# Kernel optimization log

Measured on AMD Instinct MI355X. Metric: run time of the kernel, lower is better.

Reference implementation:

```python
import jax, jax.numpy as jnp
import numpy as np

N_NODES = 50000
N_EDGES = 800000
D_IN, D_HID, D_OUT = 128, 256, 128


def setup_inputs() -> dict:
    key = jax.random.key(0)
    ks = jax.random.split(key, 8)
    x = jax.random.normal(ks[0], (N_NODES, D_IN), dtype=jnp.float32)
    edge_index = jax.random.randint(ks[1], (2, N_EDGES), 0, N_NODES, dtype=jnp.int64)
    # Xavier-ish scale for stability
    W_l1 = jax.random.normal(ks[2], (D_HID, D_IN), dtype=jnp.float32) * (1.0 / np.sqrt(D_IN))
    b_l1 = jnp.zeros((D_HID,), dtype=jnp.float32)
    W_r1 = jax.random.normal(ks[3], (D_HID, D_IN), dtype=jnp.float32) * (1.0 / np.sqrt(D_IN))
    W_l2 = jax.random.normal(ks[4], (D_OUT, D_HID), dtype=jnp.float32) * (1.0 / np.sqrt(D_HID))
    b_l2 = jnp.zeros((D_OUT,), dtype=jnp.float32)
    W_r2 = jax.random.normal(ks[5], (D_OUT, D_HID), dtype=jnp.float32) * (1.0 / np.sqrt(D_HID))
    return {"x": x, "edge_index": edge_index, "W_l1": W_l1, "b_l1": b_l1,
            "W_r1": W_r1, "W_l2": W_l2, "b_l2": b_l2, "W_r2": W_r2}


def _sage_conv(x, src, dst, W_l, b_l, W_r):
    # SAGEConv (aggr='mean', root_weight=True, normalize=False):
    #   out_i = W_l @ mean_{j in N(i)} x_j + b_l + W_r @ x_i
    n = x.shape[0]
    msgs = x[src]                                             # [E, d] gather
    agg = jax.ops.segment_sum(msgs, dst, num_segments=n)      # [N, d] scatter-add
    deg = jax.ops.segment_sum(jnp.ones((src.shape[0],), x.dtype), dst,
                              num_segments=n)
    agg = agg / jnp.maximum(deg, 1.0)[:, None]                # mean (0 for isolated)
    return agg @ W_l.T + b_l + x @ W_r.T


def reference(x, edge_index, W_l1, b_l1, W_r1, W_l2, b_l2, W_r2):
    # Note: PyG BasicGNN with num_layers=1 and jk=None applies NO activation
    # after its single conv, so the stack is two bare SAGEConv layers.
    src, dst = edge_index[0], edge_index[1]
    h = _sage_conv(x, src, dst, W_l1, b_l1, W_r1)
    out = _sage_conv(h, src, dst, W_l2, b_l2, W_r2)
    return out
```

## Files before the change

### kernel.cpp

```cpp
#include <hip/hip_runtime.h>

typedef __attribute__((ext_vector_type(4))) float f32x4;
typedef __attribute__((ext_vector_type(8))) short bf16x8;

__device__ inline ushort f2bf(float f) {
    uint u = __builtin_bit_cast(uint, f);
    u += 0x7fff + ((u >> 16) & 1);
    return (ushort)(u >> 16);
}
__device__ inline float bf2f(ushort h) {
    uint u = ((uint)h) << 16;
    return __builtin_bit_cast(float, u);
}

#define GRP 8
#define NSLICE 6250
#define CHUNK 2048

__global__ __launch_bounds__(256) void k_hist_p(const int* __restrict__ ei,
                                                int* __restrict__ cnt, int nE) {
    const int g = blockIdx.x & 7;
    const int c = blockIdx.x >> 3;
    const int lo = g * NSLICE, hi = lo + NSLICE;
    #pragma unroll
    for (int p = 0; p < CHUNK / 256; ++p) {
        int e = c * CHUNK + p * 256 + threadIdx.x;
        if (e < nE) {
            int d = ei[nE + e];
            if (d >= lo && d < hi) atomicAdd(&cnt[d], 1);
        }
    }
}

__global__ __launch_bounds__(1024) void k_scan1(const int* __restrict__ cnt,
                                                int* __restrict__ rp,
                                                int* __restrict__ bsum, int n) {
    __shared__ int buf[1024];
    const int tid = threadIdx.x;
    const int i = blockIdx.x * 1024 + tid;
    int v = (i < n) ? cnt[i] : 0;
    buf[tid] = v;
    __syncthreads();
    #pragma unroll
    for (int off = 1; off < 1024; off <<= 1) {
        int t = 0;
        if (tid >= off) t = buf[tid - off];
        __syncthreads();
        if (tid >= off) buf[tid] += t;
        __syncthreads();
    }
    if (i < n) rp[i] = buf[tid] - v;
    if (tid == 1023) bsum[blockIdx.x] = buf[1023];
}

__global__ void k_scan2(const int* __restrict__ bsum, int* __restrict__ bofs,
                        int* __restrict__ rp, int nb, int n) {
    if (threadIdx.x == 0 && blockIdx.x == 0) {
        int run = 0;
        for (int b = 0; b < nb; ++b) { bofs[b] = run; run += bsum[b]; }
        rp[n] = run;
    }
}

__global__ __launch_bounds__(1024) void k_scan3(int* __restrict__ rp,
                                                const int* __restrict__ bofs, int n) {
    int i = blockIdx.x * 1024 + threadIdx.x;
    if (i < n) rp[i] += bofs[blockIdx.x];
}

__global__ __launch_bounds__(256) void k_fill_p(const int* __restrict__ ei,
                                                const int* __restrict__ rp,
                                                int* __restrict__ cur,
                                                int* __restrict__ srt, int nE) {
    const int g = blockIdx.x & 7;
    const int c = blockIdx.x >> 3;
    const int lo = g * NSLICE, hi = lo + NSLICE;
    #pragma unroll
    for (int p = 0; p < CHUNK / 256; ++p) {
        int e = c * CHUNK + p * 256 + threadIdx.x;
        if (e < nE) {
            int d = ei[nE + e];
            int s = ei[e];
            if (d >= lo && d < hi) {
                int pos = rp[d] + atomicAdd(&cur[d], 1);
                srt[pos] = s;
            }
        }
    }
}

__global__ __launch_bounds__(256) void k_cvt_x(const float* __restrict__ x,
                                               ushort* __restrict__ A1, int n) {
    int e4 = blockIdx.x * 256 + threadIdx.x;
    if (e4 >= n * 32) return;
    int i = e4 >> 5, c4 = e4 & 31;
    float4 v = *(const float4*)(x + (size_t)i * 128 + c4 * 4);
    ushort4 o;
    o.x = f2bf(v.x); o.y = f2bf(v.y); o.z = f2bf(v.z); o.w = f2bf(v.w);
    *(ushort4*)(A1 + (size_t)i * 256 + 128 + c4 * 4) = o;
}

__global__ __launch_bounds__(256) void k_cvt_w(
    const float* __restrict__ Wl1, const float* __restrict__ Wr1,
    const float* __restrict__ Wl2, const float* __restrict__ Wr2,
    ushort* __restrict__ W1cat, ushort* __restrict__ W2cat) {
    int t = blockIdx.x * 256 + threadIdx.x;
    int which = t >> 14;
    int r = (t >> 6) & 255;
    int kq = t & 63;
    const float* src;
    ushort* dst;
    if (which == 0) {
        src = (kq < 32) ? (Wl1 + (size_t)r * 128 + kq * 4)
                        : (Wr1 + (size_t)r * 128 + (kq - 32) * 4);
        dst = W1cat + (size_t)r * 256 + kq * 4;
    } else {
        src = (r < 128) ? (Wl2 + (size_t)r * 256 + kq * 4)
                        : (Wr2 + (size_t)(r - 128) * 256 + kq * 4);
        dst = W2cat + (size_t)r * 256 + kq * 4;
    }
    float4 v = *(const float4*)src;
    ushort4 o;
    o.x = f2bf(v.x); o.y = f2bf(v.y); o.z = f2bf(v.z); o.w = f2bf(v.w);
    *(ushort4*)dst = o;
}

__global__ __launch_bounds__(256) void k_gather1(ushort* A1,
                                                 const int* __restrict__ srt,
                                                 const int* __restrict__ rp, int n) {
    const int node = blockIdx.x * 4 + (threadIdx.x >> 6);
    if (node >= n) return;
    const int lane = threadIdx.x & 63;
    const int beg = rp[node], end = rp[node + 1];
    float ax = 0.f, ay = 0.f;
    int e = beg;
    for (; e + 7 < end; e += 8) {
        uint v[8];
        #pragma unroll
        for (int q = 0; q < 8; ++q)
            v[q] = *(const uint*)(A1 + (size_t)srt[e + q] * 256 + 128 + lane * 2);
        #pragma unroll
        for (int q = 0; q < 8; ++q) {
            ax += bf2f((ushort)v[q]);
            ay += bf2f((ushort)(v[q] >> 16));
        }
    }
    for (; e < end; ++e) {
        uint v0 = *(const uint*)(A1 + (size_t)srt[e] * 256 + 128 + lane * 2);
        ax += bf2f((ushort)v0);
        ay += bf2f((ushort)(v0 >> 16));
    }
    const float invd = 1.0f / fmaxf((float)(end - beg), 1.0f);
    uint o = ((uint)f2bf(ay * invd) << 16) | (uint)f2bf(ax * invd);
    *(uint*)(A1 + (size_t)node * 256 + lane * 2) = o;
}

__global__ __launch_bounds__(256) void k_gather2(const ushort* __restrict__ H2,
                                                 const int* __restrict__ srt,
                                                 const int* __restrict__ rp,
                                                 const float* __restrict__ b2,
                                                 float* __restrict__ out, int n) {
    const int node = blockIdx.x * 4 + (threadIdx.x >> 6);
    if (node >= n) return;
    const int lane = threadIdx.x & 63;
    const int beg = rp[node], end = rp[node + 1];
    float ax = 0.f, ay = 0.f;
    int e = beg;
    for (; e + 7 < end; e += 8) {
        uint v[8];
        #pragma unroll
        for (int q = 0; q < 8; ++q)
            v[q] = *(const uint*)(H2 + (size_t)srt[e + q] * 256 + lane * 2);
        #pragma unroll
        for (int q = 0; q < 8; ++q) {
            ax += bf2f((ushort)v[q]);
            ay += bf2f((ushort)(v[q] >> 16));
        }
    }
    for (; e < end; ++e) {
        uint v0 = *(const uint*)(H2 + (size_t)srt[e] * 256 + lane * 2);
        ax += bf2f((ushort)v0);
        ay += bf2f((ushort)(v0 >> 16));
    }
    const float invd = 1.0f / fmaxf((float)(end - beg), 1.0f);
    uint rv = *(const uint*)(H2 + (size_t)node * 256 + 128 + lane * 2);
    float2 bb = *(const float2*)(b2 + lane * 2);
    float2 res;
    res.x = ax * invd + bf2f((ushort)rv) + bb.x;
    res.y = ay * invd + bf2f((ushort)(rv >> 16)) + bb.y;
    *(float2*)(out + (size_t)node * 128 + lane * 2) = res;
}

__global__ __launch_bounds__(512, 4) void k_gemm_fused(
    const ushort* __restrict__ A, const ushort* __restrict__ W1,
    const ushort* __restrict__ W2, const float* __restrict__ b1,
    ushort* __restrict__ O, int n)
{
    __shared__ __align__(16) char sA[32768];
    __shared__ __align__(16) char sH[32768];
    const int bi = blockIdx.x * 64;
    const int tid = threadIdx.x;

    #pragma unroll
    for (int p = 0; p < 4; ++p) {
        const int o = p * 8192 + tid * 16;
        const int row = o >> 9;
        const int cb = o & 511;
        uint4 v = *(const uint4*)((const char*)A + (size_t)(bi + row) * 512 + cb);
        *(uint4*)(sA + row * 512 + (cb ^ ((row & 7) << 4))) = v;
    }
    __syncthreads();

    const int wid = tid >> 6;
    const int lane = tid & 63;
    const int wn = wid * 32;
    const int lr = lane & 15;
    const int lkb = (lane >> 4) * 16;
    const int crow0 = (lane >> 4) * 4;
    const int ccol = lane & 15;

    {
        f32x4 acc[4][2] = {};
        #pragma unroll
        for (int kk = 0; kk < 8; ++kk) {
            bf16x8 wf[2], af[4];
            #pragma unroll
            for (int ni = 0; ni < 2; ++ni)
                wf[ni] = *(const bf16x8*)((const char*)W1 + (size_t)(wn + ni * 16 + lr) * 512 + kk * 64 + lkb);
            #pragma unroll
            for (int mi = 0; mi < 4; ++mi) {
                const int row = mi * 16 + lr;
                af[mi] = *(const bf16x8*)(sA + row * 512 + ((kk * 64 + lkb) ^ ((row & 7) << 4)));
            }
            #pragma unroll
            for (int mi = 0; mi < 4; ++mi)
                #pragma unroll
                for (int ni = 0; ni < 2; ++ni)
                    acc[mi][ni] = __builtin_amdgcn_mfma_f32_16x16x32_bf16(
                        af[mi], wf[ni], acc[mi][ni], 0, 0, 0);
        }
        const float badd0 = b1[wn + ccol];
        const float badd1 = b1[wn + 16 + ccol];
        #pragma unroll
        for (int mi = 0; mi < 4; ++mi)
            #pragma unroll
            for (int ni = 0; ni < 2; ++ni) {
                const int col = wn + ni * 16 + ccol;
                const float badd = ni ? badd1 : badd0;
                #pragma unroll
                for (int j = 0; j < 4; ++j) {
                    const int row = mi * 16 + crow0 + j;
                    *(ushort*)(sH + row * 512 + ((col * 2) ^ ((row & 7) << 4))) =
                        f2bf(acc[mi][ni][j] + badd);
                }
            }
    }
    __syncthreads();

    {
        f32x4 acc[4][2] = {};
        #pragma unroll
        for (int kk = 0; kk < 8; ++kk) {
            bf16x8 wf[2], af[4];
            #pragma unroll
            for (int ni = 0; ni < 2; ++ni)
                wf[ni] = *(const bf16x8*)((const char*)W2 + (size_t)(wn + ni * 16 + lr) * 512 + kk * 64 + lkb);
            #pragma unroll
            for (int mi = 0; mi < 4; ++mi) {
                const int row = mi * 16 + lr;
                af[mi] = *(const bf16x8*)(sH + row * 512 + ((kk * 64 + lkb) ^ ((row & 7) << 4)));
            }
            #pragma unroll
            for (int mi = 0; mi < 4; ++mi)
                #pragma unroll
                for (int ni = 0; ni < 2; ++ni)
                    acc[mi][ni] = __builtin_amdgcn_mfma_f32_16x16x32_bf16(
                        af[mi], wf[ni], acc[mi][ni], 0, 0, 0);
        }
        #pragma unroll
        for (int mi = 0; mi < 4; ++mi)
            #pragma unroll
            for (int ni = 0; ni < 2; ++ni) {
                const int ocol = wn + ni * 16 + ccol;
                #pragma unroll
                for (int j = 0; j < 4; ++j) {
                    const int grow = bi + mi * 16 + crow0 + j;
                    if (grow < n)
                        O[(size_t)grow * 256 + ocol] = f2bf(acc[mi][ni][j]);
                }
            }
    }
}

extern "C" void kernel_launch(void* const* d_in, const int* in_sizes, int n_in,
                              void* d_out, int out_size, void* d_ws, size_t ws_size,
                              hipStream_t stream) {
    const float* x   = (const float*)d_in[0];
    const int*   ei  = (const int*)  d_in[1];
    const float* Wl1 = (const float*)d_in[2];
    const float* bl1 = (const float*)d_in[3];
    const float* Wr1 = (const float*)d_in[4];
    const float* Wl2 = (const float*)d_in[5];
    const float* bl2 = (const float*)d_in[6];
    const float* Wr2 = (const float*)d_in[7];
    float* out = (float*)d_out;

    const int nN = 50000;
    const int nE = in_sizes[1] / 2;

    char* ws = (char*)d_ws;
    int*    rp    = (int*)   (ws);
    int*    cnt   = (int*)   (ws + 262144);
    int*    cur   = (int*)   (ws + 524288);
    int*    bsum  = (int*)   (ws + 786432);
    int*    bofs  = (int*)   (ws + 790528);
    int*    srt   = (int*)   (ws + (size_t)1 * (1 << 20));
    ushort* W1cat = (ushort*)(ws + (size_t)5 * (1 << 20));
    ushort* W2cat = (ushort*)(ws + (size_t)5 * (1 << 20) + 256 * 1024);
    ushort* A1    = (ushort*)(ws + (size_t)6 * (1 << 20));
    ushort* H2    = (ushort*)(ws + (size_t)32 * (1 << 20));

    const int nb = (nN + 1023) / 1024;
    const int nChunks = (nE + CHUNK - 1) / CHUNK;

    hipMemsetAsync(ws + 262144, 0, 462144, stream);
    k_hist_p<<<nChunks * GRP, 256, 0, stream>>>(ei, cnt, nE);
    k_scan1<<<nb, 1024, 0, stream>>>(cnt, rp, bsum, nN);
    k_scan2<<<1, 64, 0, stream>>>(bsum, bofs, rp, nb, nN);
    k_scan3<<<nb, 1024, 0, stream>>>(rp, bofs, nN);
    k_fill_p<<<nChunks * GRP, 256, 0, stream>>>(ei, rp, cur, srt, nE);

    k_cvt_x<<<(nN * 32 + 255) / 256, 256, 0, stream>>>(x, A1, nN);
    k_cvt_w<<<128, 256, 0, stream>>>(Wl1, Wr1, Wl2, Wr2, W1cat, W2cat);

    k_gather1<<<(nN + 3) / 4, 256, 0, stream>>>(A1, srt, rp, nN);
    k_gemm_fused<<<(nN + 63) / 64, 512, 0, stream>>>(A1, W1cat, W2cat, bl1, H2, nN);

    k_gather2<<<(nN + 3) / 4, 256, 0, stream>>>(H2, srt, rp, bl2, out, nN);
}
```

Baseline: 294.5 us.

## Fuse preprocessing kernels, merge scans, widen gathers, and share GEMM LDS buffer

Merges x/weight conversion and the histogram into one launch, and folds the serial block-offset scan into the add pass using a wave shuffle scan. The gathers now have each lane load 16 bytes and process four edges per wave-iteration, with cross-quad shuffle reductions. The fused GEMM reuses one LDS buffer for both stages so occupancy can rise from 4 to 6 blocks. The fill kernel loads the source index only when the edge is in range. These changes aim to cut launch overhead, serial scan latency and memory transaction count, at the cost of extra shuffles and masked lanes for low-degree nodes.

```diff
diff --git a/kernel.cpp b/kernel.cpp
--- a/kernel.cpp
+++ b/kernel.cpp
@@ -12,15 +12,59 @@
     uint u = ((uint)h) << 16;
     return __builtin_bit_cast(float, u);
 }
+__device__ inline uint packbf(float lo, float hi) {
+    return (uint)f2bf(lo) | ((uint)f2bf(hi) << 16);
+}
 
 #define GRP 8
 #define NSLICE 6250
 #define CHUNK 2048
 
-__global__ __launch_bounds__(256) void k_hist_p(const int* __restrict__ ei,
-                                                int* __restrict__ cnt, int nE) {
-    const int g = blockIdx.x & 7;
-    const int c = blockIdx.x >> 3;
+__global__ __launch_bounds__(256) void k_pre(
+    const float* __restrict__ x,
+    const float* __restrict__ Wl1, const float* __restrict__ Wr1,
+    const float* __restrict__ Wl2, const float* __restrict__ Wr2,
+    const int* __restrict__ ei,
+    ushort* __restrict__ A1, ushort* __restrict__ W1cat, ushort* __restrict__ W2cat,
+    int* __restrict__ cnt, int n, int nE, int nxb, int histBase)
+{
+    const int b = blockIdx.x;
+    if (b < nxb) {
+        int e4 = b * 256 + threadIdx.x;
+        if (e4 >= n * 32) return;
+        int i = e4 >> 5, c4 = e4 & 31;
+        float4 v = *(const float4*)(x + (size_t)i * 128 + c4 * 4);
+        ushort4 o;
+        o.x = f2bf(v.x); o.y = f2bf(v.y); o.z = f2bf(v.z); o.w = f2bf(v.w);
+        *(ushort4*)(A1 + (size_t)i * 256 + 128 + c4 * 4) = o;
+        return;
+    }
+    if (b < nxb + 128) {
+        int t = (b - nxb) * 256 + threadIdx.x;
+        int which = t >> 14;
+        int r = (t >> 6) & 255;
+        int kq = t & 63;
+        const float* src;
+        ushort* dst;
+        if (which == 0) {
+            src = (kq < 32) ? (Wl1 + (size_t)r * 128 + kq * 4)
+                            : (Wr1 + (size_t)r * 128 + (kq - 32) * 4);
+            dst = W1cat + (size_t)r * 256 + kq * 4;
+        } else {
+            src = (r < 128) ? (Wl2 + (size_t)r * 256 + kq * 4)
+                            : (Wr2 + (size_t)(r - 128) * 256 + kq * 4);
+            dst = W2cat + (size_t)r * 256 + kq * 4;
+        }
+        float4 v = *(const float4*)src;
+        ushort4 o;
+        o.x = f2bf(v.x); o.y = f2bf(v.y); o.z = f2bf(v.z); o.w = f2bf(v.w);
+        *(ushort4*)dst = o;
+        return;
+    }
+    if (b < histBase) return;
+    const int hb = b - histBase;
+    const int g = hb & 7;
+    const int c = hb >> 3;
     const int lo = g * NSLICE, hi = lo + NSLICE;
     #pragma unroll
     for (int p = 0; p < CHUNK / 256; ++p) {
@@ -53,19 +97,25 @@
     if (tid == 1023) bsum[blockIdx.x] = buf[1023];
 }
 
-__global__ void k_scan2(const int* __restrict__ bsum, int* __restrict__ bofs,
-                        int* __restrict__ rp, int nb, int n) {
-    if (threadIdx.x == 0 && blockIdx.x == 0) {
-        int run = 0;
-        for (int b = 0; b < nb; ++b) { bofs[b] = run; run += bsum[b]; }
-        rp[n] = run;
-    }
-}
-
-__global__ __launch_bounds__(1024) void k_scan3(int* __restrict__ rp,
-                                                const int* __restrict__ bofs, int n) {
+__global__ __launch_bounds__(1024) void k_scan3b(int* __restrict__ rp,
+                                                 const int* __restrict__ bsum,
+                                                 int nb, int n) {
+    __shared__ int sofs;
+    if (threadIdx.x < 64) {
+        int i = threadIdx.x;
+        int v = (i < nb) ? bsum[i] : 0;
+        int s = v;
+        #pragma unroll
+        for (int off = 1; off < 64; off <<= 1) {
+            int t = __shfl_up(s, off, 64);
+            if (i >= off) s += t;
+        }
+        if (i == (int)blockIdx.x) sofs = s - v;
+        if ((int)blockIdx.x == nb - 1 && i == nb - 1) rp[n] = s;
+    }
+    __syncthreads();
     int i = blockIdx.x * 1024 + threadIdx.x;
-    if (i < n) rp[i] += bofs[blockIdx.x];
+    if (i < n) rp[i] += sofs;
 }
 
 __global__ __launch_bounds__(256) void k_fill_p(const int* __restrict__ ei,
@@ -80,49 +130,13 @@
         int e = c * CHUNK + p * 256 + threadIdx.x;
         if (e < nE) {
             int d = ei[nE + e];
-            int s = ei[e];
             if (d >= lo && d < hi) {
+                int s = ei[e];
                 int pos = rp[d] + atomicAdd(&cur[d], 1);
                 srt[pos] = s;
             }
         }
     }
-}
-
-__global__ __launch_bounds__(256) void k_cvt_x(const float* __restrict__ x,
-                                               ushort* __restrict__ A1, int n) {
-    int e4 = blockIdx.x * 256 + threadIdx.x;
-    if (e4 >= n * 32) return;
-    int i = e4 >> 5, c4 = e4 & 31;
-    float4 v = *(const float4*)(x + (size_t)i * 128 + c4 * 4);
-    ushort4 o;
-    o.x = f2bf(v.x); o.y = f2bf(v.y); o.z = f2bf(v.z); o.w = f2bf(v.w);
-    *(ushort4*)(A1 + (size_t)i * 256 + 128 + c4 * 4) = o;
-}
-
-__global__ __launch_bounds__(256) void k_cvt_w(
-    const float* __restrict__ Wl1, const float* __restrict__ Wr1,
-    const float* __restrict__ Wl2, const float* __restrict__ Wr2,
-    ushort* __restrict__ W1cat, ushort* __restrict__ W2cat) {
-    int t = blockIdx.x * 256 + threadIdx.x;
-    int which = t >> 14;
-    int r = (t >> 6) & 255;
-    int kq = t & 63;
-    const float* src;
-    ushort* dst;
-    if (which == 0) {
-        src = (kq < 32) ? (Wl1 + (size_t)r * 128 + kq * 4)
-                        : (Wr1 + (size_t)r * 128 + (kq - 32) * 4);
-        dst = W1cat + (size_t)r * 256 + kq * 4;
-    } else {
-        src = (r < 128) ? (Wl2 + (size_t)r * 256 + kq * 4)
-                        : (Wr2 + (size_t)(r - 128) * 256 + kq * 4);
-        dst = W2cat + (size_t)r * 256 + kq * 4;
-    }
-    float4 v = *(const float4*)src;
-    ushort4 o;
-    o.x = f2bf(v.x); o.y = f2bf(v.y); o.z = f2bf(v.z); o.w = f2bf(v.w);
-    *(ushort4*)dst = o;
 }
 
 __global__ __launch_bounds__(256) void k_gather1(ushort* A1,
@@ -131,28 +145,47 @@
     const int node = blockIdx.x * 4 + (threadIdx.x >> 6);
     if (node >= n) return;
     const int lane = threadIdx.x & 63;
+    const int quad = lane >> 4;
+    const int col16 = (lane & 15) * 16;
     const int beg = rp[node], end = rp[node + 1];
-    float ax = 0.f, ay = 0.f;
-    int e = beg;
-    for (; e + 7 < end; e += 8) {
-        uint v[8];
-        #pragma unroll
-        for (int q = 0; q < 8; ++q)
-            v[q] = *(const uint*)(A1 + (size_t)srt[e + q] * 256 + 128 + lane * 2);
-        #pragma unroll
-        for (int q = 0; q < 8; ++q) {
-            ax += bf2f((ushort)v[q]);
-            ay += bf2f((ushort)(v[q] >> 16));
-        }
-    }
-    for (; e < end; ++e) {
-        uint v0 = *(const uint*)(A1 + (size_t)srt[e] * 256 + 128 + lane * 2);
-        ax += bf2f((ushort)v0);
-        ay += bf2f((ushort)(v0 >> 16));
-    }
-    const float invd = 1.0f / fmaxf((float)(end - beg), 1.0f);
-    uint o = ((uint)f2bf(ay * invd) << 16) | (uint)f2bf(ax * invd);
-    *(uint*)(A1 + (size_t)node * 256 + lane * 2) = o;
+    float a0 = 0.f, a1 = 0.f, a2 = 0.f, a3 = 0.f;
+    float a4 = 0.f, a5 = 0.f, a6 = 0.f, a7 = 0.f;
+    for (int e = beg; e < end; e += 16) {
+        uint4 v[4]; int live[4];
+        #pragma unroll
+        for (int q = 0; q < 4; ++q) {
+            int idx = e + q * 4 + quad;
+            live[q] = idx < end;
+            int s = srt[live[q] ? idx : end - 1];
+            v[q] = *(const uint4*)((const char*)A1 + (size_t)s * 512 + 256 + col16);
+        }
+        #pragma unroll
+        for (int q = 0; q < 4; ++q) {
+            if (live[q]) {
+                a0 += bf2f((ushort)v[q].x);  a1 += bf2f((ushort)(v[q].x >> 16));
+                a2 += bf2f((ushort)v[q].y);  a3 += bf2f((ushort)(v[q].y >> 16));
+                a4 += bf2f((ushort)v[q].z);  a5 += bf2f((ushort)(v[q].z >> 16));
+                a6 += bf2f((ushort)v[q].w);  a7 += bf2f((ushort)(v[q].w >> 16));
+            }
+        }
+    }
+    a0 += __shfl_xor(a0, 16); a1 += __shfl_xor(a1, 16);
+    a2 += __shfl_xor(a2, 16); a3 += __shfl_xor(a3, 16);
+    a4 += __shfl_xor(a4, 16); a5 += __shfl_xor(a5, 16);
+    a6 += __shfl_xor(a6, 16); a7 += __shfl_xor(a7, 16);
+    a0 += __shfl_xor(a0, 32); a1 += __shfl_xor(a1, 32);
+    a2 += __shfl_xor(a2, 32); a3 += __shfl_xor(a3, 32);
+    a4 += __shfl_xor(a4, 32); a5 += __shfl_xor(a5, 32);
+    a6 += __shfl_xor(a6, 32); a7 += __shfl_xor(a7, 32);
+    if (quad == 0) {
+        const float invd = 1.0f / fmaxf((float)(end - beg), 1.0f);
+        uint4 o;
+        o.x = packbf(a0 * invd, a1 * invd);
+        o.y = packbf(a2 * invd, a3 * invd);
+        o.z = packbf(a4 * invd, a5 * invd);
+        o.w = packbf(a6 * invd, a7 * invd);
+        *(uint4*)((char*)A1 + (size_t)node * 512 + col16) = o;
+    }
 }
 
 __global__ __launch_bounds__(256) void k_gather2(const ushort* __restrict__ H2,
@@ -163,41 +196,64 @@
     const int node = blockIdx.x * 4 + (threadIdx.x >> 6);
     if (node >= n) return;
     const int lane = threadIdx.x & 63;
+    const int quad = lane >> 4;
+    const int col16 = (lane & 15) * 16;
     const int beg = rp[node], end = rp[node + 1];
-    float ax = 0.f, ay = 0.f;
-    int e = beg;
-    for (; e + 7 < end; e += 8) {
-        uint v[8];
-        #pragma unroll
-        for (int q = 0; q < 8; ++q)
-            v[q] = *(const uint*)(H2 + (size_t)srt[e + q] * 256 + lane * 2);
-        #pragma unroll
-        for (int q = 0; q < 8; ++q) {
-            ax += bf2f((ushort)v[q]);
-            ay += bf2f((ushort)(v[q] >> 16));
-        }
-    }
-    for (; e < end; ++e) {
-        uint v0 = *(const uint*)(H2 + (size_t)srt[e] * 256 + lane * 2);
-        ax += bf2f((ushort)v0);
-        ay += bf2f((ushort)(v0 >> 16));
-    }
-    const float invd = 1.0f / fmaxf((float)(end - beg), 1.0f);
-    uint rv = *(const uint*)(H2 + (size_t)node * 256 + 128 + lane * 2);
-    float2 bb = *(const float2*)(b2 + lane * 2);
-    float2 res;
-    res.x = ax * invd + bf2f((ushort)rv) + bb.x;
-    res.y = ay * invd + bf2f((ushort)(rv >> 16)) + bb.y;
-    *(float2*)(out + (size_t)node * 128 + lane * 2) = res;
-}
-
-__global__ __launch_bounds__(512, 4) void k_gemm_fused(
+    float a0 = 0.f, a1 = 0.f, a2 = 0.f, a3 = 0.f;
+    float a4 = 0.f, a5 = 0.f, a6 = 0.f, a7 = 0.f;
+    for (int e = beg; e < end; e += 16) {
+        uint4 v[4]; int live[4];
+        #pragma unroll
+        for (int q = 0; q < 4; ++q) {
+            int idx = e + q * 4 + quad;
+            live[q] = idx < end;
+            int s = srt[live[q] ? idx : end - 1];
+            v[q] = *(const uint4*)((const char*)H2 + (size_t)s * 512 + col16);
+        }
+        #pragma unroll
+        for (int q = 0; q < 4; ++q) {
+            if (live[q]) {
+                a0 += bf2f((ushort)v[q].x);  a1 += bf2f((ushort)(v[q].x >> 16));
+                a2 += bf2f((ushort)v[q].y);  a3 += bf2f((ushort)(v[q].y >> 16));
+                a4 += bf2f((ushort)v[q].z);  a5 += bf2f((ushort)(v[q].z >> 16));
+                a6 += bf2f((ushort)v[q].w);  a7 += bf2f((ushort)(v[q].w >> 16));
+            }
+        }
+    }
+    a0 += __shfl_xor(a0, 16); a1 += __shfl_xor(a1, 16);
+    a2 += __shfl_xor(a2, 16); a3 += __shfl_xor(a3, 16);
+    a4 += __shfl_xor(a4, 16); a5 += __shfl_xor(a5, 16);
+    a6 += __shfl_xor(a6, 16); a7 += __shfl_xor(a7, 16);
+    a0 += __shfl_xor(a0, 32); a1 += __shfl_xor(a1, 32);
+    a2 += __shfl_xor(a2, 32); a3 += __shfl_xor(a3, 32);
+    a4 += __shfl_xor(a4, 32); a5 += __shfl_xor(a5, 32);
+    a6 += __shfl_xor(a6, 32); a7 += __shfl_xor(a7, 32);
+    if (quad == 0) {
+        const float invd = 1.0f / fmaxf((float)(end - beg), 1.0f);
+        uint4 rv = *(const uint4*)((const char*)H2 + (size_t)node * 512 + 256 + col16);
+        const int c8 = (lane & 15) * 8;
+        float4 bb0 = *(const float4*)(b2 + c8);
+        float4 bb1 = *(const float4*)(b2 + c8 + 4);
+        float4 r0, r1;
+        r0.x = a0 * invd + bf2f((ushort)rv.x) + bb0.x;
+        r0.y = a1 * invd + bf2f((ushort)(rv.x >> 16)) + bb0.y;
+        r0.z = a2 * invd + bf2f((ushort)rv.y) + bb0.z;
+        r0.w = a3 * invd + bf2f((ushort)(rv.y >> 16)) + bb0.w;
+        r1.x = a4 * invd + bf2f((ushort)rv.z) + bb1.x;
+        r1.y = a5 * invd + bf2f((ushort)(rv.z >> 16)) + bb1.y;
+        r1.z = a6 * invd + bf2f((ushort)rv.w) + bb1.z;
+        r1.w = a7 * invd + bf2f((ushort)(rv.w >> 16)) + bb1.w;
+        *(float4*)(out + (size_t)node * 128 + c8) = r0;
+        *(float4*)(out + (size_t)node * 128 + c8 + 4) = r1;
+    }
+}
+
+__global__ __launch_bounds__(512, 6) void k_gemm_fused(
     const ushort* __restrict__ A, const ushort* __restrict__ W1,
     const ushort* __restrict__ W2, const float* __restrict__ b1,
     ushort* __restrict__ O, int n)
 {
     __shared__ __align__(16) char sA[32768];
-    __shared__ __align__(16) char sH[32768];
     const int bi = blockIdx.x * 64;
     const int tid = threadIdx.x;
 
@@ -219,26 +275,28 @@
     const int crow0 = (lane >> 4) * 4;
     const int ccol = lane & 15;
 
+    f32x4 acc[4][2] = {};
+    #pragma unroll
+    for (int kk = 0; kk < 8; ++kk) {
+        bf16x8 wf[2], af[4];
+        #pragma unroll
+        for (int ni = 0; ni < 2; ++ni)
+            wf[ni] = *(const bf16x8*)((const char*)W1 + (size_t)(wn + ni * 16 + lr) * 512 + kk * 64 + lkb);
+        #pragma unroll
+        for (int mi = 0; mi < 4; ++mi) {
+            const int row = mi * 16 + lr;
+            af[mi] = *(const bf16x8*)(sA + row * 512 + ((kk * 64 + lkb) ^ ((row & 7) << 4)));
+        }
+        #pragma unroll
+        for (int mi = 0; mi < 4; ++mi)
+            #pragma unroll
+            for (int ni = 0; ni < 2; ++ni)
+                acc[mi][ni] = __builtin_amdgcn_mfma_f32_16x16x32_bf16(
+                    af[mi], wf[ni], acc[mi][ni], 0, 0, 0);
+    }
+    __syncthreads();
+
     {
-        f32x4 acc[4][2] = {};
-        #pragma unroll
-        for (int kk = 0; kk < 8; ++kk) {
-            bf16x8 wf[2], af[4];
-            #pragma unroll
-            for (int ni = 0; ni < 2; ++ni)
-                wf[ni] = *(const bf16x8*)((const char*)W1 + (size_t)(wn + ni * 16 + lr) * 512 + kk * 64 + lkb);
-            #pragma unroll
-            for (int mi = 0; mi < 4; ++mi) {
-                const int row = mi * 16 + lr;
-                af[mi] = *(const bf16x8*)(sA + row * 512 + ((kk * 64 + lkb) ^ ((row & 7) << 4)));
-            }
-            #pragma unroll
-            for (int mi = 0; mi < 4; ++mi)
-                #pragma unroll
-                for (int ni = 0; ni < 2; ++ni)
-                    acc[mi][ni] = __builtin_amdgcn_mfma_f32_16x16x32_bf16(
-                        af[mi], wf[ni], acc[mi][ni], 0, 0, 0);
-        }
         const float badd0 = b1[wn + ccol];
         const float badd1 = b1[wn + 16 + ccol];
         #pragma unroll
@@ -250,7 +308,7 @@
                 #pragma unroll
                 for (int j = 0; j < 4; ++j) {
                     const int row = mi * 16 + crow0 + j;
-                    *(ushort*)(sH + row * 512 + ((col * 2) ^ ((row & 7) << 4))) =
+                    *(ushort*)(sA + row * 512 + ((col * 2) ^ ((row & 7) << 4))) =
                         f2bf(acc[mi][ni][j] + badd);
                 }
             }
@@ -258,7 +316,7 @@
     __syncthreads();
 
     {
-        f32x4 acc[4][2] = {};
+        f32x4 acc2[4][2] = {};
         #pragma unroll
         for (int kk = 0; kk < 8; ++kk) {
             bf16x8 wf[2], af[4];
@@ -268,14 +326,14 @@
             #pragma unroll
             for (int mi = 0; mi < 4; ++mi) {
                 const int row = mi * 16 + lr;
-                af[mi] = *(const bf16x8*)(sH + row * 512 + ((kk * 64 + lkb) ^ ((row & 7) << 4)));
+                af[mi] = *(const bf16x8*)(sA + row * 512 + ((kk * 64 + lkb) ^ ((row & 7) << 4)));
             }
             #pragma unroll
             for (int mi = 0; mi < 4; ++mi)
                 #pragma unroll
                 for (int ni = 0; ni < 2; ++ni)
-                    acc[mi][ni] = __builtin_amdgcn_mfma_f32_16x16x32_bf16(
-                        af[mi], wf[ni], acc[mi][ni], 0, 0, 0);
+                    acc2[mi][ni] = __builtin_amdgcn_mfma_f32_16x16x32_bf16(
+                        af[mi], wf[ni], acc2[mi][ni], 0, 0, 0);
         }
         #pragma unroll
         for (int mi = 0; mi < 4; ++mi)
@@ -286,7 +344,7 @@
                 for (int j = 0; j < 4; ++j) {
                     const int grow = bi + mi * 16 + crow0 + j;
                     if (grow < n)
-                        O[(size_t)grow * 256 + ocol] = f2bf(acc[mi][ni][j]);
+                        O[(size_t)grow * 256 + ocol] = f2bf(acc2[mi][ni][j]);
                 }
             }
     }
@@ -313,28 +371,27 @@
     int*    cnt   = (int*)   (ws + 262144);
     int*    cur   = (int*)   (ws + 524288);
     int*    bsum  = (int*)   (ws + 786432);
-    int*    bofs  = (int*)   (ws + 790528);
     int*    srt   = (int*)   (ws + (size_t)1 * (1 << 20));
     ushort* W1cat = (ushort*)(ws + (size_t)5 * (1 << 20));
-    ushort* W2cat = (ushort*)(ws + (size_t)5 * (1 << 20) + 256 * 1024);
+    ushort* W2cat = (ushort*)(ws + (size_t)5 * (1 << 20) + 262144);
     ushort* A1    = (ushort*)(ws + (size_t)6 * (1 << 20));
     ushort* H2    = (ushort*)(ws + (size_t)32 * (1 << 20));
 
     const int nb = (nN + 1023) / 1024;
     const int nChunks = (nE + CHUNK - 1) / CHUNK;
-
-    hipMemsetAsync(ws + 262144, 0, 462144, stream);
-    k_hist_p<<<nChunks * GRP, 256, 0, stream>>>(ei, cnt, nE);
+    const int nxb = (nN * 32 + 255) / 256;
+    const int histBase = (nxb + 128 + 7) & ~7;
+
+    hipMemsetAsync(cnt, 0, 524288, stream);
+
+    k_pre<<<histBase + nChunks * GRP, 256, 0, stream>>>(
+        x, Wl1, Wr1, Wl2, Wr2, ei, A1, W1cat, W2cat, cnt, nN, nE, nxb, histBase);
+
     k_scan1<<<nb, 1024, 0, stream>>>(cnt, rp, bsum, nN);
-    k_scan2<<<1, 64, 0, stream>>>(bsum, bofs, rp, nb, nN);
-    k_scan3<<<nb, 1024, 0, stream>>>(rp, bofs, nN);
+    k_scan3b<<<nb, 1024, 0, stream>>>(rp, bsum, nb, nN);
     k_fill_p<<<nChunks * GRP, 256, 0, stream>>>(ei, rp, cur, srt, nE);
-
-    k_cvt_x<<<(nN * 32 + 255) / 256, 256, 0, stream>>>(x, A1, nN);
-    k_cvt_w<<<128, 256, 0, stream>>>(Wl1, Wr1, Wl2, Wr2, W1cat, W2cat);
 
     k_gather1<<<(nN + 3) / 4, 256, 0, stream>>>(A1, srt, rp, nN);
     k_gemm_fused<<<(nN + 63) / 64, 512, 0, stream>>>(A1, W1cat, W2cat, bl1, H2, nN);
-
     k_gather2<<<(nN + 3) / 4, 256, 0, stream>>>(H2, srt, rp, bl2, out, nN);
 }
```

After: 269.7 us. 1.09x faster.
